# Kernel optimization log

Hardware: AMD Instinct MI355X
Metric: run time of the kernel (lower is better)

The kernel has to match this reference:

```python
import jax, jax.numpy as jnp
import numpy as np
import math

N_EMBD = 1024
N_HEAD = 16
D_HEAD = N_EMBD // N_HEAD
LCOMP = 576 // 2  # 288
B, T = 4, 2048

def setup_inputs() -> dict:
    key = jax.random.key(0)
    k1, k2, k3, k4 = jax.random.split(key, 4)
    x = jax.random.normal(k1, (B, T, N_EMBD), dtype=jnp.float32)
    Wdkv = jax.random.normal(k2, (B, T, LCOMP), dtype=jnp.float32)
    # nn.Linear(n_embd, LCompression): weight [LCOMP, n_embd], bias [LCOMP]
    Wd_w = jax.random.normal(k3, (LCOMP, N_EMBD), dtype=jnp.float32) * (1.0 / math.sqrt(N_EMBD))
    Wd_b = jax.random.normal(k4, (LCOMP,), dtype=jnp.float32) * 0.01
    return {"x": x, "Wdkv": Wdkv, "Wd_w": Wd_w, "Wd_b": Wd_b}

def reference(x, Wdkv, Wd_w, Wd_b):
    b, t, c = x.shape
    # q: [b, t, LCOMP]
    q = jnp.einsum('btc,lc->btl', x, Wd_w) + Wd_b
    # scores: [b, t, t] -- query positions attend over latent rows of Wdkv
    h = jnp.einsum('btl,bsl->bts', q, Wdkv) / math.sqrt(D_HEAD)
    causal = jnp.tril(jnp.ones((t, t), dtype=bool))  # True where allowed
    h = jnp.where(causal[None, :, :], h, -jnp.inf)
    y = jax.nn.softmax(h, axis=-1)
    # output: [b, t, LCOMP]
    return jnp.einsum('bts,bsl->btl', y, Wdkv)
```

## Files before the change

kernel.cpp:

```cpp
#include <hip/hip_runtime.h>

#define TT 2048
#define LL 288
#define CC 1024
#define SLOTB2 74752

typedef __attribute__((ext_vector_type(8))) short bf16x8;
typedef __attribute__((ext_vector_type(4))) float f32x4;
typedef __attribute__((ext_vector_type(4))) unsigned int u32x4;
typedef __attribute__((ext_vector_type(2))) unsigned int u32x2;
typedef __attribute__((ext_vector_type(4))) short s16x4;

__device__ __forceinline__ unsigned short f2bf(float f) {
  unsigned u = __float_as_uint(f);
  u += 0x7fffu + ((u >> 16) & 1u);
  return (unsigned short)(u >> 16);
}

__device__ __forceinline__ u32x2 pack4(f32x4 v) {
  u32x2 p;
  p.x = (unsigned)f2bf(v.x) | ((unsigned)f2bf(v.y) << 16);
  p.y = (unsigned)f2bf(v.z) | ((unsigned)f2bf(v.w) << 16);
  return p;
}

__device__ __forceinline__ f32x4 mfma16(bf16x8 a, bf16x8 b, f32x4 c) {
  return __builtin_amdgcn_mfma_f32_16x16x32_bf16(a, b, c, 0, 0, 0);
}

__device__ __forceinline__ bf16x8 as_bf(u32x4 u) {
  return __builtin_bit_cast(bf16x8, u);
}

__device__ __forceinline__ unsigned cvtpk(float lo, float hi) {
  unsigned d;
  asm("v_cvt_pk_bf16_f32 %0, %1, %2" : "=v"(d) : "v"(lo), "v"(hi));
  return d;
}

typedef __attribute__((address_space(3))) const unsigned short* lds_cptr;
typedef __attribute__((address_space(1))) const void* gvp;
typedef __attribute__((address_space(3))) void* svp;

__device__ __forceinline__ s16x4 tr16(const void* p) {
  s16x4 r;
  lds_cptr lp = (lds_cptr)p;
  asm volatile("ds_read_b64_tr_b16 %0, %1" : "=v"(r) : "v"(lp));
  return r;
}

__device__ __forceinline__ void gll16(const void* g, void* l) {
  __builtin_amdgcn_global_load_lds((gvp)g, (svp)l, 16, 0, 0);
}

__global__ __launch_bounds__(256) void tobf16(const float* __restrict__ wdkv,
                                              const float* __restrict__ ww,
                                              unsigned short* __restrict__ wdkvT,
                                              unsigned short* __restrict__ wwB) {
  long i8 = (long)blockIdx.x * 256 + threadIdx.x;
  if (i8 < 36864L) {
    long k = i8;
    f32x4 a = *(const f32x4*)(ww + k * 8);
    f32x4 c = *(const f32x4*)(ww + k * 8 + 4);
    u32x2 p0 = pack4(a), p1 = pack4(c);
    u32x4 o;
    o.x = p0.x; o.y = p0.y; o.z = p1.x; o.w = p1.y;
    *(u32x4*)(wwB + k * 8) = o;
  } else {
    long k = i8 - 36864L;
    int b = (int)(k / 73728);
    int rem = (int)(k % 73728);
    int srow = rem / 36;
    int l8 = rem - srow * 36;
    int st = srow >> 6;
    int s = srow & 63;
    int j = (l8 >> 1) * 2 + (s >> 5);
    int lane = ((s & 31) >> 2) * 8 + (s & 3) * 2 + (l8 & 1);
    f32x4 a = *(const f32x4*)(wdkv + k * 8);
    f32x4 c = *(const f32x4*)(wdkv + k * 8 + 4);
    u32x2 p0 = pack4(a), p1 = pack4(c);
    u32x4 o;
    o.x = p0.x; o.y = p0.y; o.z = p1.x; o.w = p1.y;
    *(u32x4*)((char*)wdkvT + (((long)(b * 32 + st) * 36 + j) << 10) + lane * 16) = o;
  }
}

__global__ __launch_bounds__(256, 4) void qproj(const float* __restrict__ x,
                                                const unsigned short* __restrict__ wwB,
                                                const float* __restrict__ Wb,
                                                unsigned short* __restrict__ q) {
  __shared__ unsigned short xl[2][64 * 64];
  __shared__ unsigned short wl[2][96 * 64];
  const int tid = threadIdx.x;
  const int lane = tid & 63;
  const int w = tid >> 6;
  const int g = lane >> 4;
  const int r = lane & 15;
  const int m0 = (blockIdx.x / 3) * 64;
  const int c0 = (blockIdx.x % 3) * 96;

  const int o_i = (lane >> 3) * 2048 + (((lane & 7) * 16) ^ ((lane >> 3) << 4));

  const int mi = tid >> 2;
  const int kq = (tid & 3) * 16;
  const float* xrow = x + (long)(m0 + mi) * CC + kq;
  const int xb0 = mi * 128 + (((kq * 2) + 0) ^ ((mi & 7) << 4));
  const int xb1 = mi * 128 + (((kq * 2) + 16) ^ ((mi & 7) << 4));

  f32x4 acc[6];
#pragma unroll
  for (int i = 0; i < 6; ++i) acc[i] = (f32x4)0.0f;

  const char* wsrc = (const char*)wwB + (long)c0 * 2048;

#define QPROJ_W_ISSUE(kb2, cb)                                          \
  {                                                                     \
    char* wd = (char*)&wl[cb][0];                                       \
    _Pragma("unroll") for (int jj = 0; jj < 3; ++jj) {                  \
      int j = 3 * w + jj;                                               \
      gll16(wsrc + (long)j * 16384 + (kb2) + o_i, wd + j * 1024);       \
    }                                                                   \
  }

  {
    f32x4 a0 = *(const f32x4*)(xrow + 0);
    f32x4 a1 = *(const f32x4*)(xrow + 4);
    f32x4 a2 = *(const f32x4*)(xrow + 8);
    f32x4 a3 = *(const f32x4*)(xrow + 12);
    QPROJ_W_ISSUE(0, 0);
    u32x2 pA = pack4(a0), pB = pack4(a1), pC = pack4(a2), pD = pack4(a3);
    u32x4 v0, v1;
    v0.x = pA.x; v0.y = pA.y; v0.z = pB.x; v0.w = pB.y;
    v1.x = pC.x; v1.y = pC.y; v1.z = pD.x; v1.w = pD.y;
    *(u32x4*)((char*)&xl[0][0] + xb0) = v0;
    *(u32x4*)((char*)&xl[0][0] + xb1) = v1;
  }
  asm volatile("s_waitcnt vmcnt(0) lgkmcnt(0)" ::: "memory");
  __builtin_amdgcn_s_barrier();
  __builtin_amdgcn_sched_barrier(0);

  for (int ks = 0; ks < 16; ++ks) {
    const int cb = ks & 1;
    f32x4 a0, a1, a2, a3;
    if (ks < 15) {
      const float* xs = xrow + (ks + 1) * 64;
      a0 = *(const f32x4*)(xs + 0);
      a1 = *(const f32x4*)(xs + 4);
      a2 = *(const f32x4*)(xs + 8);
      a3 = *(const f32x4*)(xs + 12);
      QPROJ_W_ISSUE((ks + 1) * 128, cb ^ 1);
    }
    const char* xlb = (const char*)&xl[cb][0];
    const char* wlb = (const char*)&wl[cb][0];
#pragma unroll
    for (int kc = 0; kc < 2; ++kc) {
      int koff = kc * 64 + g * 16;
      bf16x8 a = as_bf(*(const u32x4*)(xlb + (16 * w + r) * 128 + (koff ^ ((r & 7) << 4))));
#pragma unroll
      for (int nf = 0; nf < 6; ++nf) {
        int l = nf * 16 + r;
        bf16x8 bb = as_bf(*(const u32x4*)(wlb + l * 128 + (koff ^ ((l & 7) << 4))));
        acc[nf] = mfma16(a, bb, acc[nf]);
      }
    }
    if (ks < 15) {
      asm volatile("s_waitcnt vmcnt(0)" ::: "memory");
      u32x2 pA = pack4(a0), pB = pack4(a1), pC = pack4(a2), pD = pack4(a3);
      u32x4 v0, v1;
      v0.x = pA.x; v0.y = pA.y; v0.z = pB.x; v0.w = pB.y;
      v1.x = pC.x; v1.y = pC.y; v1.z = pD.x; v1.w = pD.y;
      char* xd = (char*)&xl[cb ^ 1][0];
      *(u32x4*)(xd + xb0) = v0;
      *(u32x4*)(xd + xb1) = v1;
    }
    asm volatile("s_waitcnt lgkmcnt(0)" ::: "memory");
    __builtin_amdgcn_sched_barrier(0);
    __builtin_amdgcn_s_barrier();
    __builtin_amdgcn_sched_barrier(0);
  }
  const int rowb = m0 + 16 * w + 4 * g;
#pragma unroll
  for (int nf = 0; nf < 6; ++nf) {
    int col = c0 + nf * 16 + r;
    float bias = Wb[col];
#pragma unroll
    for (int e = 0; e < 4; ++e) {
      float qv = (acc[nf][e] + bias) * 0.125f;
      q[(long)(rowb + e) * LL + col] = f2bf(qv);
    }
  }
}

__global__ __launch_bounds__(512, 2) void attn(const unsigned short* __restrict__ wdkvT,
                                               const unsigned short* __restrict__ q,
                                               float* __restrict__ out,
                                               char* __restrict__ partial,
                                               int CH, int SPB) {
  __shared__ unsigned short Vt[2][18 * 16 * 64];
  const int tid = threadIdx.x;
  const int lane = tid & 63;
  const int w = tid >> 6;
  const int g = lane >> 4;
  const int r = lane & 15;

  const int bid = blockIdx.x;
  const int b = bid / SPB;
  int rem = bid - b * SPB;
  int t = 0, base = 0, nch = 1;
  for (;;) {
    nch = (2 * t + 2 + CH - 1) / CH;
    if (rem < base + nch) break;
    base += nch;
    ++t;
  }
  const int c = rem - base;
  const bool direct = (nch == 1);
  const int q0 = t * 128;
  const int st0 = c * CH;
  const int st1 = min((c + 1) * CH, 2 * t + 2);

  char* vt0 = (char*)&Vt[0][0];
  char* vt1 = (char*)&Vt[1][0];

  const char* wsrcT = (const char*)wdkvT + (long)b * 32 * 36864;

  bf16x8 qf[9];
  {
    const long qrow = (long)b * TT + q0 + 16 * w + r;
#pragma unroll
    for (int kc = 0; kc < 9; ++kc)
      qf[kc] = as_bf(*(const u32x4*)(q + qrow * LL + kc * 32 + 8 * g));
  }

  f32x4 o[18];
#pragma unroll
  for (int i = 0; i < 18; ++i) o[i] = (f32x4)0.0f;
  float mr = -1e30f, lr = 0.0f;

#define ATTN_ISSUE(st_, dst_)                                          \
  {                                                                    \
    const char* srcT = wsrcT + (long)(st_) * 36864;                    \
    _Pragma("unroll") for (int jj = 0; jj < 5; ++jj) {                 \
      int j = w + 8 * jj;                                              \
      if (j < 36) gll16(srcT + j * 1024 + lane * 16, (dst_) + j * 1024);\
    }                                                                  \
  }

  const int rq = q0 + 16 * w + r;
  const int srcA = r + 32 * (g & 1);
  const int srcB = srcA + 16;
  const bool gsel = (g & 2) != 0;

  ATTN_ISSUE(st0, vt0);
  for (int st = st0; st < st1; ++st) {
    const int sb = st * 64;
    const int cbi = (st - st0) & 1;
    char* vtb = cbi ? vt1 : vt0;
    char* vtn = cbi ? vt0 : vt1;
    asm volatile("s_waitcnt vmcnt(0)" ::: "memory");
    __builtin_amdgcn_s_barrier();
    __builtin_amdgcn_sched_barrier(0);
    if (st + 1 < st1) ATTN_ISSUE(st + 1, vtn);
    f32x4 sa[4];
#pragma unroll
    for (int i = 0; i < 4; ++i) sa[i] = (f32x4)0.0f;
    __builtin_amdgcn_s_setprio(1);
#pragma unroll
    for (int kc = 0; kc < 9; ++kc) {
      const int lblk2048 = (2 * kc + (g >> 1)) * 2048;
      const int lrem16 = (g & 1) * 16;
#pragma unroll
      for (int sf = 0; sf < 4; ++sf) {
        bf16x8 vv = as_bf(*(const u32x4*)(vtb + lblk2048 + (4 * sf + (r >> 2)) * 128 + (r & 3) * 32 + lrem16));
        sa[sf] = mfma16(vv, qf[kc], sa[sf]);
      }
    }
    __builtin_amdgcn_s_setprio(0);
    float tm = -1e30f;
#pragma unroll
    for (int sf = 0; sf < 4; ++sf)
#pragma unroll
      for (int e = 0; e < 4; ++e) {
        int sg = sb + 16 * sf + 4 * g + e;
        if (sg > rq) sa[sf][e] = -1e30f;
        tm = fmaxf(tm, sa[sf][e]);
      }
    tm = fmaxf(tm, __shfl_xor(tm, 16));
    tm = fmaxf(tm, __shfl_xor(tm, 32));
    const float mn = fmaxf(mr, tm);
    const float al = __expf(mr - mn);
    mr = mn;
    float rs = 0.0f;
#pragma unroll
    for (int sf = 0; sf < 4; ++sf)
#pragma unroll
      for (int e = 0; e < 4; ++e) {
        float pv = __expf(sa[sf][e] - mn);
        sa[sf][e] = pv;
        rs += pv;
      }
    rs += __shfl_xor(rs, 16);
    rs += __shfl_xor(rs, 32);
    lr = lr * al + rs;
    float alr[4];
#pragma unroll
    for (int e = 0; e < 4; ++e) alr[e] = __shfl(al, 4 * g + e);
#pragma unroll
    for (int nf = 0; nf < 18; ++nf)
#pragma unroll
      for (int e = 0; e < 4; ++e) o[nf][e] *= alr[e];
    unsigned pk[4][2];
#pragma unroll
    for (int sf = 0; sf < 4; ++sf) {
      pk[sf][0] = cvtpk(sa[sf][0], sa[sf][1]);
      pk[sf][1] = cvtpk(sa[sf][2], sa[sf][3]);
    }
    bf16x8 paK0, paK1;
#pragma unroll
    for (int kc2 = 0; kc2 < 2; ++kc2) {
      int xa0 = __shfl((int)pk[2 * kc2 + 0][0], srcA);
      int xb0 = __shfl((int)pk[2 * kc2 + 1][0], srcA);
      int xa1 = __shfl((int)pk[2 * kc2 + 0][1], srcA);
      int xb1 = __shfl((int)pk[2 * kc2 + 1][1], srcA);
      int ya0 = __shfl((int)pk[2 * kc2 + 0][0], srcB);
      int yb0 = __shfl((int)pk[2 * kc2 + 1][0], srcB);
      int ya1 = __shfl((int)pk[2 * kc2 + 0][1], srcB);
      int yb1 = __shfl((int)pk[2 * kc2 + 1][1], srcB);
      u32x4 pd;
      pd.x = (unsigned)(gsel ? xb0 : xa0);
      pd.y = (unsigned)(gsel ? xb1 : xa1);
      pd.z = (unsigned)(gsel ? yb0 : ya0);
      pd.w = (unsigned)(gsel ? yb1 : ya1);
      if (kc2 == 0) paK0 = as_bf(pd); else paK1 = as_bf(pd);
    }
    asm volatile("" : "+v"(paK0), "+v"(paK1));
    s16x4 tq[3][2];
#define PV_ISSUE(c_, sl_)                                                   \
    {                                                                       \
      const char* ap = vtb + ((c_) % 18) * 2048 + ((c_) / 18) * 1024 + g * 256 + r * 8; \
      tq[sl_][0] = tr16(ap);                                                \
      tq[sl_][1] = tr16(ap + 128);                                          \
    }
    __builtin_amdgcn_s_setprio(1);
    PV_ISSUE(0, 0);
    PV_ISSUE(1, 1);
#pragma unroll
    for (int cc2 = 0; cc2 < 36; ++cc2) {
      if (cc2 < 34) {
        PV_ISSUE(cc2 + 2, (cc2 + 2) % 3);
        asm volatile("s_waitcnt lgkmcnt(4)" ::: "memory");
      } else if (cc2 == 34) {
        asm volatile("s_waitcnt lgkmcnt(2)" ::: "memory");
      } else {
        asm volatile("s_waitcnt lgkmcnt(0)" ::: "memory");
      }
      __builtin_amdgcn_sched_barrier(0);
      const int nf = cc2 % 18;
      s16x4 t0 = tq[cc2 % 3][0], t1 = tq[cc2 % 3][1];
      bf16x8 bb;
      bb[0] = t0[0]; bb[1] = t0[1]; bb[2] = t0[2]; bb[3] = t0[3];
      bb[4] = t1[0]; bb[5] = t1[1]; bb[6] = t1[2]; bb[7] = t1[3];
      o[nf] = mfma16((cc2 < 18) ? paK0 : paK1, bb, o[nf]);
    }
    __builtin_amdgcn_s_setprio(0);
  }
  if (direct) {
    float lrr[4];
#pragma unroll
    for (int e = 0; e < 4; ++e) lrr[e] = __shfl(lr, 4 * g + e);
    const long trow = (long)b * TT + q0 + 16 * w + 4 * g;
#pragma unroll
    for (int nf = 0; nf < 18; ++nf) {
      int col = 16 * nf + r;
#pragma unroll
      for (int e = 0; e < 4; ++e)
        out[(trow + e) * LL + col] = o[nf][e] / lrr[e];
    }
  } else {
    char* sp = partial + (size_t)(b * SPB + rem) * SLOTB2;
    if (g == 0) {
      ((float*)sp)[16 * w + r] = mr;
      ((float*)(sp + 512))[16 * w + r] = lr;
    }
#pragma unroll
    for (int p = 0; p < 9; ++p) {
      u32x2 a0 = pack4(o[2 * p]);
      u32x2 a1 = pack4(o[2 * p + 1]);
      u32x4 v;
      v.x = a0.x; v.y = a0.y; v.z = a1.x; v.w = a1.y;
      *(u32x4*)(sp + 1024 + p * 8192 + tid * 16) = v;
    }
  }
}

__global__ __launch_bounds__(512) void reduce_k(const char* __restrict__ partial,
                                                float* __restrict__ out,
                                                int CH, int SPB, int NMT) {
  const int bid = blockIdx.x;
  const int nfl = bid % 9;
  const int rest = bid / 9;
  const int b = rest / NMT;
  int idx = rest % NMT;
  int t = 0, base = 0, nch = 1;
  for (;;) {
    nch = (2 * t + 2 + CH - 1) / CH;
    if (nch > 1) {
      if (idx == 0) break;
      --idx;
    }
    base += nch;
    ++t;
  }
  const char* sp0 = partial + (size_t)(b * SPB + base) * SLOTB2;

  const int tid = threadIdx.x;
  const int w = tid >> 6;
  const int g = (tid & 63) >> 4;
  const int r = tid & 15;
  const int row0 = 16 * w + 4 * g;

  float M[4], Lx[4], acc[8];
#pragma unroll
  for (int e = 0; e < 4; ++e) { M[e] = -1e30f; Lx[e] = 0.0f; }
#pragma unroll
  for (int k = 0; k < 8; ++k) acc[k] = 0.0f;

  for (int i = 0; i < nch; ++i) {
    const char* sp = sp0 + (size_t)i * SLOTB2;
    const float* mv = (const float*)sp;
    const float* lv = (const float*)(sp + 512);
    u32x4 v = *(const u32x4*)(sp + 1024 + nfl * 8192 + tid * 16);
    const unsigned short* pu = (const unsigned short*)&v;
    float fo[4], fi[4];
#pragma unroll
    for (int e = 0; e < 4; ++e) {
      float mi = mv[row0 + e];
      float mn = fmaxf(M[e], mi);
      fo[e] = __expf(M[e] - mn);
      fi[e] = __expf(mi - mn);
      Lx[e] = Lx[e] * fo[e] + fi[e] * lv[row0 + e];
      M[e] = mn;
    }
#pragma unroll
    for (int k = 0; k < 8; ++k)
      acc[k] = acc[k] * fo[k & 3] + fi[k & 3] * __uint_as_float((unsigned)pu[k] << 16);
  }
#pragma unroll
  for (int k = 0; k < 8; ++k) {
    int row = row0 + (k & 3);
    int col = 16 * (2 * nfl + (k >> 2)) + r;
    out[((size_t)b * TT + t * 128 + row) * LL + col] = acc[k] / Lx[k & 3];
  }
}

extern "C" void kernel_launch(void* const* d_in, const int* in_sizes, int n_in,
                              void* d_out, int out_size, void* d_ws, size_t ws_size,
                              hipStream_t stream) {
  const float* x = (const float*)d_in[0];
  const float* Wdkv = (const float*)d_in[1];
  const float* Ww = (const float*)d_in[2];
  const float* Wb = (const float*)d_in[3];
  float* outp = (float*)d_out;

  char* ws = (char*)d_ws;
  unsigned short* qB = (unsigned short*)ws;
  unsigned short* wdkvT = (unsigned short*)(ws + 4718592);
  unsigned short* wwB = (unsigned short*)(ws + 9437184);
  char* partialB = ws + 10027008;

  int CH = 32, SPB = 16;
  const int chs[4] = {5, 8, 16, 32};
  for (int ci = 0; ci < 4; ++ci) {
    int ch = chs[ci];
    int spb = 0;
    for (int t = 0; t < 16; ++t) spb += (2 * t + 2 + ch - 1) / ch;
    if (10027008 + (size_t)4 * spb * SLOTB2 <= ws_size) { CH = ch; SPB = spb; break; }
  }
  int NMT = 0;
  for (int t = 0; t < 16; ++t)
    if ((2 * t + 2 + CH - 1) / CH > 1) ++NMT;

  tobf16<<<1296, 256, 0, stream>>>(Wdkv, Ww, wdkvT, wwB);
  qproj<<<384, 256, 0, stream>>>(x, wwB, Wb, qB);
  attn<<<4 * SPB, 512, 0, stream>>>(wdkvT, qB, outp, partialB, CH, SPB);
  if (NMT > 0) reduce_k<<<4 * NMT * 9, 512, 0, stream>>>(partialB, outp, CH, SPB, NMT);
}
```

Before: 70.67 us.

## Triple-buffer qproj weight loads and regroup PV transpose-read batching

In the q projection, the weight tile staging moves from double to triple buffering, so weight loads are issued two k-steps ahead and the wait only drains the older batch (vmcnt(3)). In the attention PV loop, the rolling 3-slot transpose-read prefetch is replaced by batches of six reads followed by a full wait and three MFMAs, per packed P fragment. This is meant to hide global load latency in qproj and simplify the PV schedule. In exchange it uses more LDS in qproj, which can lower occupancy, and the PV batches now drain lgkmcnt fully before each group of MFMAs.

```diff
diff --git a/kernel.cpp b/kernel.cpp
--- a/kernel.cpp
+++ b/kernel.cpp
@@ -90,7 +90,7 @@
                                                 const float* __restrict__ Wb,
                                                 unsigned short* __restrict__ q) {
   __shared__ unsigned short xl[2][64 * 64];
-  __shared__ unsigned short wl[2][96 * 64];
+  __shared__ unsigned short wl[3][96 * 64];
   const int tid = threadIdx.x;
   const int lane = tid & 63;
   const int w = tid >> 6;
@@ -113,13 +113,23 @@
 
   const char* wsrc = (const char*)wwB + (long)c0 * 2048;
 
-#define QPROJ_W_ISSUE(kb2, cb)                                          \
+#define QPROJ_W_ISSUE(kb2, bufi)                                        \
   {                                                                     \
-    char* wd = (char*)&wl[cb][0];                                       \
+    char* wd = (char*)&wl[bufi][0];                                     \
     _Pragma("unroll") for (int jj = 0; jj < 3; ++jj) {                  \
       int j = 3 * w + jj;                                               \
       gll16(wsrc + (long)j * 16384 + (kb2) + o_i, wd + j * 1024);       \
     }                                                                   \
+  }
+
+#define QPROJ_X_WRITE(dstb)                                             \
+  {                                                                     \
+    u32x2 pA = pack4(a0), pB = pack4(a1), pC = pack4(a2), pD = pack4(a3); \
+    u32x4 v0, v1;                                                       \
+    v0.x = pA.x; v0.y = pA.y; v0.z = pB.x; v0.w = pB.y;                 \
+    v1.x = pC.x; v1.y = pC.y; v1.z = pD.x; v1.w = pD.y;                 \
+    *(u32x4*)((dstb) + xb0) = v0;                                       \
+    *(u32x4*)((dstb) + xb1) = v1;                                       \
   }
 
   {
@@ -128,14 +138,11 @@
     f32x4 a2 = *(const f32x4*)(xrow + 8);
     f32x4 a3 = *(const f32x4*)(xrow + 12);
     QPROJ_W_ISSUE(0, 0);
-    u32x2 pA = pack4(a0), pB = pack4(a1), pC = pack4(a2), pD = pack4(a3);
-    u32x4 v0, v1;
-    v0.x = pA.x; v0.y = pA.y; v0.z = pB.x; v0.w = pB.y;
-    v1.x = pC.x; v1.y = pC.y; v1.z = pD.x; v1.w = pD.y;
-    *(u32x4*)((char*)&xl[0][0] + xb0) = v0;
-    *(u32x4*)((char*)&xl[0][0] + xb1) = v1;
-  }
-  asm volatile("s_waitcnt vmcnt(0) lgkmcnt(0)" ::: "memory");
+    QPROJ_W_ISSUE(128, 1);
+    asm volatile("s_waitcnt vmcnt(6)" ::: "memory");
+    QPROJ_X_WRITE((char*)&xl[0][0]);
+    asm volatile("s_waitcnt vmcnt(3) lgkmcnt(0)" ::: "memory");
+  }
   __builtin_amdgcn_s_barrier();
   __builtin_amdgcn_sched_barrier(0);
 
@@ -148,10 +155,10 @@
       a1 = *(const f32x4*)(xs + 4);
       a2 = *(const f32x4*)(xs + 8);
       a3 = *(const f32x4*)(xs + 12);
-      QPROJ_W_ISSUE((ks + 1) * 128, cb ^ 1);
-    }
+    }
+    if (ks < 14) QPROJ_W_ISSUE((ks + 2) * 128, (ks + 2) % 3);
     const char* xlb = (const char*)&xl[cb][0];
-    const char* wlb = (const char*)&wl[cb][0];
+    const char* wlb = (const char*)&wl[ks % 3][0];
 #pragma unroll
     for (int kc = 0; kc < 2; ++kc) {
       int koff = kc * 64 + g * 16;
@@ -164,14 +171,13 @@
       }
     }
     if (ks < 15) {
-      asm volatile("s_waitcnt vmcnt(0)" ::: "memory");
-      u32x2 pA = pack4(a0), pB = pack4(a1), pC = pack4(a2), pD = pack4(a3);
-      u32x4 v0, v1;
-      v0.x = pA.x; v0.y = pA.y; v0.z = pB.x; v0.w = pB.y;
-      v1.x = pC.x; v1.y = pC.y; v1.z = pD.x; v1.w = pD.y;
+      if (ks < 14) {
+        asm volatile("s_waitcnt vmcnt(3)" ::: "memory");
+      } else {
+        asm volatile("s_waitcnt vmcnt(0)" ::: "memory");
+      }
       char* xd = (char*)&xl[cb ^ 1][0];
-      *(u32x4*)(xd + xb0) = v0;
-      *(u32x4*)(xd + xb1) = v1;
+      QPROJ_X_WRITE(xd);
     }
     asm volatile("s_waitcnt lgkmcnt(0)" ::: "memory");
     __builtin_amdgcn_sched_barrier(0);
@@ -315,7 +321,6 @@
       pk[sf][0] = cvtpk(sa[sf][0], sa[sf][1]);
       pk[sf][1] = cvtpk(sa[sf][2], sa[sf][3]);
     }
-    bf16x8 paK0, paK1;
 #pragma unroll
     for (int kc2 = 0; kc2 < 2; ++kc2) {
       int xa0 = __shfl((int)pk[2 * kc2 + 0][0], srcA);
@@ -331,38 +336,32 @@
       pd.y = (unsigned)(gsel ? xb1 : xa1);
       pd.z = (unsigned)(gsel ? yb0 : ya0);
       pd.w = (unsigned)(gsel ? yb1 : ya1);
-      if (kc2 == 0) paK0 = as_bf(pd); else paK1 = as_bf(pd);
-    }
-    asm volatile("" : "+v"(paK0), "+v"(paK1));
-    s16x4 tq[3][2];
-#define PV_ISSUE(c_, sl_)                                                   \
-    {                                                                       \
-      const char* ap = vtb + ((c_) % 18) * 2048 + ((c_) / 18) * 1024 + g * 256 + r * 8; \
-      tq[sl_][0] = tr16(ap);                                                \
-      tq[sl_][1] = tr16(ap + 128);                                          \
-    }
-    __builtin_amdgcn_s_setprio(1);
-    PV_ISSUE(0, 0);
-    PV_ISSUE(1, 1);
-#pragma unroll
-    for (int cc2 = 0; cc2 < 36; ++cc2) {
-      if (cc2 < 34) {
-        PV_ISSUE(cc2 + 2, (cc2 + 2) % 3);
-        asm volatile("s_waitcnt lgkmcnt(4)" ::: "memory");
-      } else if (cc2 == 34) {
-        asm volatile("s_waitcnt lgkmcnt(2)" ::: "memory");
-      } else {
+      bf16x8 pa = as_bf(pd);
+      const int base0 = kc2 * 1024 + g * 256 + r * 8;
+#pragma unroll
+      for (int gg = 0; gg < 6; ++gg) {
+        s16x4 tq[6];
+#pragma unroll
+        for (int i = 0; i < 3; ++i) {
+          int nf = gg * 3 + i;
+          tq[2 * i] = tr16(vtb + nf * 2048 + base0);
+          tq[2 * i + 1] = tr16(vtb + nf * 2048 + base0 + 128);
+        }
         asm volatile("s_waitcnt lgkmcnt(0)" ::: "memory");
-      }
-      __builtin_amdgcn_sched_barrier(0);
-      const int nf = cc2 % 18;
-      s16x4 t0 = tq[cc2 % 3][0], t1 = tq[cc2 % 3][1];
-      bf16x8 bb;
-      bb[0] = t0[0]; bb[1] = t0[1]; bb[2] = t0[2]; bb[3] = t0[3];
-      bb[4] = t1[0]; bb[5] = t1[1]; bb[6] = t1[2]; bb[7] = t1[3];
-      o[nf] = mfma16((cc2 < 18) ? paK0 : paK1, bb, o[nf]);
-    }
-    __builtin_amdgcn_s_setprio(0);
+        __builtin_amdgcn_sched_barrier(0);
+        __builtin_amdgcn_s_setprio(1);
+#pragma unroll
+        for (int i = 0; i < 3; ++i) {
+          int nf = gg * 3 + i;
+          s16x4 t0 = tq[2 * i], t1 = tq[2 * i + 1];
+          bf16x8 bb;
+          bb[0] = t0[0]; bb[1] = t0[1]; bb[2] = t0[2]; bb[3] = t0[3];
+          bb[4] = t1[0]; bb[5] = t1[1]; bb[6] = t1[2]; bb[7] = t1[3];
+          o[nf] = mfma16(pa, bb, o[nf]);
+        }
+        __builtin_amdgcn_s_setprio(0);
+      }
+    }
   }
   if (direct) {
     float lrr[4];
```

Result: faster. 68.57 us (-3.0%).
